# Kernel tuning notes

Measured on AMD Instinct MI355X. Metric: run time of the kernel, lower is better.

Reference implementation:

```python
import jax, jax.numpy as jnp
import numpy as np
from jax import lax

EPS = 1e-5
B, NV, NP, C = 1, 12000, 32, 5
VF = 128            # voxel_feat_dim
OF = 256            # output_feat_dim
D0, H0, W0 = 16, 128, 128


def _bn(x, gamma, beta, axes):
    # training-mode batch norm (biased variance), channel dim broadcasts via gamma/beta shape
    mean = jnp.mean(x, axis=axes, keepdims=True)
    var = jnp.var(x, axis=axes, keepdims=True)
    return (x - mean) * lax.rsqrt(var + EPS) * gamma + beta


def _vfe(x, w, b, gamma, beta):
    # x: (B, NVox, NPts, Cin) -> (B, NVox, Cout); linear -> BN1d over all rows -> relu -> max over points
    y = jnp.einsum('bvpc,co->bvpo', x, w) + b
    Bv, Nv, Pp, Co = y.shape
    y = _bn(y.reshape(Bv * Nv * Pp, Co), gamma, beta, axes=0).reshape(Bv, Nv, Pp, Co)
    y = jax.nn.relu(y)
    return jnp.max(y, axis=2)


def _conv_bn_relu(x, w, b, gamma, beta):
    y = lax.conv_general_dilated(x, w, (2, 2, 2), [(1, 1)] * 3,
                                 dimension_numbers=('NCDHW', 'OIDHW', 'NCDHW'))
    y = y + b[None, :, None, None, None]
    y = _bn(y, gamma[None, :, None, None, None], beta[None, :, None, None, None], axes=(0, 2, 3, 4))
    return jax.nn.relu(y)


def setup_inputs() -> dict:
    key = jax.random.key(0)
    ks = jax.random.split(key, 20)
    vf = VF // 2
    inp = {
        'voxel_features': jax.random.normal(ks[0], (B, NV, NP, C), jnp.float32),
        'voxel_coords': jnp.stack([
            jax.random.randint(ks[1], (B, NV), 0, D0),
            jax.random.randint(ks[2], (B, NV), 0, H0),
            jax.random.randint(ks[3], (B, NV), 0, W0)], axis=-1).astype(jnp.int32),
        'grid_d': D0, 'grid_h': H0, 'grid_w': W0,
        # VFE1: 5 -> 64
        'w1': jax.random.normal(ks[4], (C, vf), jnp.float32) * 0.05,
        'b1': jnp.zeros((vf,), jnp.float32),
        'g1': jnp.ones((vf,), jnp.float32),
        'be1': jnp.zeros((vf,), jnp.float32),
        # VFE2: 64 -> 128
        'w2': jax.random.normal(ks[5], (vf, VF), jnp.float32) * 0.05,
        'b2': jnp.zeros((VF,), jnp.float32),
        'g2': jnp.ones((VF,), jnp.float32),
        'be2': jnp.zeros((VF,), jnp.float32),
        # conv3d stack
        'cw1': jax.random.normal(ks[6], (128, VF, 3, 3, 3), jnp.float32) * 0.02,
        'cb1': jnp.zeros((128,), jnp.float32),
        'cg1': jnp.ones((128,), jnp.float32),
        'cbe1': jnp.zeros((128,), jnp.float32),
        'cw2': jax.random.normal(ks[7], (256, 128, 3, 3, 3), jnp.float32) * 0.02,
        'cb2': jnp.zeros((256,), jnp.float32),
        'cg2': jnp.ones((256,), jnp.float32),
        'cbe2': jnp.zeros((256,), jnp.float32),
        'cw3': jax.random.normal(ks[8], (OF, 256, 3, 3, 3), jnp.float32) * 0.02,
        'cb3': jnp.zeros((OF,), jnp.float32),
        'cg3': jnp.ones((OF,), jnp.float32),
        'cbe3': jnp.zeros((OF,), jnp.float32),
    }
    return inp


def reference(voxel_features, voxel_coords, grid_d, grid_h, grid_w,
              w1, b1, g1, be1, w2, b2, g2, be2,
              cw1, cb1, cg1, cbe1, cw2, cb2, cg2, cbe2, cw3, cb3, cg3, cbe3):
    # VFE1: (B, NV, NP, C) -> (B, NV, 64)
    f = _vfe(voxel_features, w1, b1, g1, be1)
    # VFE2 (repaired: singleton points dim, max over 1 point is identity)
    f = _vfe(f[:, :, None, :], w2, b2, g2, be2)  # (B, NV, 128)

    Bn, Nn, Cf = f.shape
    grid = jnp.zeros((Bn, grid_d, grid_h, grid_w, Cf), f.dtype)
    bidx = jnp.broadcast_to(jnp.arange(Bn)[:, None], (Bn, Nn))
    grid = grid.at[bidx, voxel_coords[..., 0], voxel_coords[..., 1], voxel_coords[..., 2]].set(f)
    grid = jnp.transpose(grid, (0, 4, 1, 2, 3))  # (B, Cf, D, H, W)

    x = _conv_bn_relu(grid, cw1, cb1, cg1, cbe1)
    x = _conv_bn_relu(x, cw2, cb2, cg2, cbe2)
    x = _conv_bn_relu(x, cw3, cb3, cg3, cbe3)
    return x
```

## Files before the change

### kernel.cpp

```cpp
#include <hip/hip_runtime.h>

#define NVOX 12000
#define NPTS 32
#define CIN  5
#define C1   64
#define C2   128
#define GD   16
#define GH   128
#define GW   128
#define SP   (GD*GH*GW)
static constexpr float EPSBN = 1e-5f;

typedef unsigned short ushortT;
typedef __attribute__((ext_vector_type(8))) short bf16x8;
typedef __attribute__((ext_vector_type(4))) float f32x4;

__device__ inline ushortT f2bf(float f) {
    unsigned int x = __float_as_uint(f);
    unsigned int r = (x + 0x7FFFu + ((x >> 16) & 1u)) >> 16;
    return (ushortT)r;
}
__device__ inline float bf2f(ushortT u) { return __uint_as_float(((unsigned int)u) << 16); }

__device__ inline void gload16(const ushortT* g, ushortT* l) {
    __builtin_amdgcn_global_load_lds(
        (const __attribute__((address_space(1))) unsigned int*)g,
        (__attribute__((address_space(3))) unsigned int*)l, 16, 0, 0);
}

#define P1D 18
#define P1H 130
#define P1W 130
#define PSP1 (P1D*P1H*P1W)
#define P2D 10
#define P2H 66
#define P2W 66
#define PSP2 (P2D*P2H*P2W)
#define P3D 6
#define P3H 34
#define P3W 34
#define PSP3 (P3D*P3H*P3W)


__device__ inline void conv_w_one(const float* cw, ushortT* wb, int CI_, int TCO_,
                                  int NS_, int e) {
    int j = e & 7;
    int rest = e >> 3;
    int CHN = TCO_*16;
    int p = rest % CHN; int r = rest / CHN;
    int s = r % NS_;    int cob = r / NS_;
    int col = p >> 4, cp = p & 15;
    int cl = cp ^ (col & 7);
    int tap = (CI_==256) ? (s>>1) : s;
    int cib = (CI_==256) ? ((s&1)*128) : 0;
    int co = cob*TCO_ + col;
    int ci = cib + cl*8 + j;
    wb[e] = f2bf(cw[((size_t)co*CI_ + ci)*27 + tap]);
}

__global__ void prep(const float* __restrict__ x, const float* __restrict__ w1,
                     float* __restrict__ s1sum,
                     const float* __restrict__ cw1, const float* __restrict__ cw2,
                     const float* __restrict__ cw3, ushortT* __restrict__ wb1,
                     ushortT* __restrict__ wb2, ushortT* __restrict__ wb3,
                     const int* __restrict__ coords, int* __restrict__ winner) {
    __shared__ float s_w[CIN*C1];
    __shared__ float s_red[2][4][C1];
    const int blk = blockIdx.x;
    const int t = threadIdx.x;
    if (blk < 960) {
        for (int i = t; i < CIN*C1; i += 256) s_w[i] = w1[i];
        __syncthreads();
        int ch = t & 63, rr = t >> 6;
        float sum = 0.f, sq = 0.f;
        const int NROWS = NVOX * NPTS;
        for (int row = blk*4 + rr; row < NROWS; row += 960*4) {
            const float* xr = x + row*CIN;
            float y = 0.f;
            #pragma unroll
            for (int c = 0; c < CIN; ++c) y += xr[c] * s_w[c*C1 + ch];
            sum += y; sq += y*y;
        }
        s_red[0][rr][ch] = sum; s_red[1][rr][ch] = sq;
        __syncthreads();
        if (rr == 0) {
            sum = s_red[0][0][ch]+s_red[0][1][ch]+s_red[0][2][ch]+s_red[0][3][ch];
            sq  = s_red[1][0][ch]+s_red[1][1][ch]+s_red[1][2][ch]+s_red[1][3][ch];
            atomicAdd(&s1sum[ch], sum);
            atomicAdd(&s1sum[C1+ch], sq);
        }
    } else if (blk < 1984) {
        const int N1 = 442368, N2 = 884736, N3 = 1769472;
        const int total = N1+N2+N3;
        for (int e0 = (blk-960)*256 + t; e0 < total; e0 += 1024*256) {
            if (e0 < N1)         conv_w_one(cw1, wb1, 128, 128, 27, e0);
            else if (e0 < N1+N2) conv_w_one(cw2, wb2, 128, 128, 27, e0-N1);
            else                 conv_w_one(cw3, wb3, 256, 64,  54, e0-N1-N2);
        }
    } else {
        int v = (blk-1984)*256 + t;
        if (v < NVOX) {
            int d = coords[v*3+0], h = coords[v*3+1], w = coords[v*3+2];
            atomicMax(&winner[(d*GH + h)*GW + w], v);
        }
    }
}

__global__ void vfe1_apply(const float* __restrict__ x, const float* __restrict__ w1,
                           const float* __restrict__ sums, const float* __restrict__ g,
                           const float* __restrict__ be, float* __restrict__ f1) {
    __shared__ float s_w[CIN*C1];
    __shared__ float s_x[4*NPTS*CIN];
    int v0 = blockIdx.x*4, t = threadIdx.x;
    for (int i = t; i < CIN*C1; i += 256) s_w[i] = w1[i];
    for (int i = t; i < 4*NPTS*CIN; i += 256) s_x[i] = x[(size_t)v0*NPTS*CIN + i];
    int sub = t >> 6, ch = t & 63;
    const float invN = 1.f/(NVOX*NPTS);
    float mean = sums[ch]*invN;
    float var  = sums[C1+ch]*invN - mean*mean;
    float sc = g[ch]*rsqrtf(var + EPSBN);
    float sh = be[ch] - mean*sc;
    __syncthreads();
    float m = 0.f;
    const float* xs = s_x + sub*NPTS*CIN;
    for (int p = 0; p < NPTS; ++p) {
        float y = 0.f;
        #pragma unroll
        for (int c = 0; c < CIN; ++c) y += xs[p*CIN+c]*s_w[c*C1+ch];
        m = fmaxf(m, y*sc + sh);
    }
    f1[(v0+sub)*C1 + ch] = m;
}

__global__ void vfe2_linear(const float* __restrict__ f1, const float* __restrict__ w2,
                            float* __restrict__ y2, float* __restrict__ sums) {
    __shared__ float s_w[C2][68];
    __shared__ float s_f[16*C1];
    int t = threadIdx.x;
    for (int i = t; i < C1*C2; i += 128) {
        int c = i >> 7, o = i & 127;
        s_w[o][c] = w2[i];
    }
    int v0 = blockIdx.x*16;
    for (int i = t; i < 16*C1; i += 128) s_f[i] = f1[v0*C1 + i];
    __syncthreads();
    float sum = 0.f, sq = 0.f;
    for (int vl = 0; vl < 16; ++vl) {
        float y = 0.f;
        #pragma unroll
        for (int c4 = 0; c4 < C1; c4 += 4) {
            float4 f = *(const float4*)&s_f[vl*C1 + c4];
            float4 w = *(const float4*)&s_w[t][c4];
            y += f.x*w.x + f.y*w.y + f.z*w.z + f.w*w.w;
        }
        y2[(v0+vl)*C2 + t] = y;
        sum += y; sq += y*y;
    }
    atomicAdd(&sums[t], sum);
    atomicAdd(&sums[C2+t], sq);
}

__global__ void vfe2_apply_bf16(const float* __restrict__ y2, const float* __restrict__ sums,
                                const float* __restrict__ g, const float* __restrict__ be,
                                ushortT* __restrict__ f2b) {
    __shared__ float s_sc[C2], s_sh[C2];
    int t = threadIdx.x;
    if (t < C2) {
        const float invN = 1.f/NVOX;
        float mean = sums[t]*invN;
        float var  = sums[C2+t]*invN - mean*mean;
        float sc = g[t]*rsqrtf(var + EPSBN);
        s_sc[t] = sc; s_sh[t] = be[t] - mean*sc;
    }
    __syncthreads();
    int i = blockIdx.x*256 + t;
    if (i >= NVOX*C2/4) return;
    const float4 v = *(const float4*)(y2 + (size_t)i*4);
    int c0 = (i*4) & (C2-1);
    ushort4 o;
    o.x = f2bf(fmaxf(0.f, v.x*s_sc[c0+0]+s_sh[c0+0]));
    o.y = f2bf(fmaxf(0.f, v.y*s_sc[c0+1]+s_sh[c0+1]));
    o.z = f2bf(fmaxf(0.f, v.z*s_sc[c0+2]+s_sh[c0+2]));
    o.w = f2bf(fmaxf(0.f, v.w*s_sc[c0+3]+s_sh[c0+3]));
    *(ushort4*)(f2b + (size_t)i*4) = o;
}

__global__ void build_grid_cl(const int* __restrict__ winner, const ushortT* __restrict__ f2b,
                              ushortT* __restrict__ grid) {
    const int total = PSP1*16;
    for (int e = blockIdx.x*256 + threadIdx.x; e < total; e += gridDim.x*256) {
        int pos = e >> 4, ch = e & 15;
        int pz = pos / (P1H*P1W); int rr = pos % (P1H*P1W);
        int py = rr / P1W; int px = rr % P1W;
        unsigned dz = pz-1, dy = py-1, dx = px-1;
        int4 v = {0,0,0,0};
        if (dz < GD && dy < GH && dx < GW) {
            int wn_ = winner[(dz*GH + dy)*GW + dx];
            if (wn_ >= 0) v = *(const int4*)(f2b + (size_t)wn_*C2 + ch*8);
        }
        *(int4*)(grid + ((size_t)pos << 7) + ch*8) = v;
    }
}

template<int CI, int CO, int TILE_CO, int TILE_SP, int THREADS,
         int PD, int PH, int PW, int DO, int HO, int WO,
         int OPH, int OPW, int NS, int NSLICE, bool ATOMIC>
__global__ __launch_bounds__(THREADS) void conv3d_mfma(
        const ushortT* __restrict__ in_p, const ushortT* __restrict__ wb,
        void* __restrict__ outp, float* __restrict__ sums_out) {
    constexpr int NW      = THREADS/64;
    constexpr int WAVES_M = TILE_CO/32;
    constexpr int WAVES_N = NW/WAVES_M;
    constexpr int FRAG_N  = TILE_SP/(WAVES_N*16);
    constexpr int TILE_Y  = TILE_SP/8;
    constexpr int SPB     = NS/NSLICE;
    constexpr int WCH     = TILE_CO*16;

    __shared__ ushortT s_x[2][TILE_SP*128];
    __shared__ ushortT s_w[2][TILE_CO*128];

    constexpr int nbx = WO/8, nby = HO/TILE_Y;
    constexpr int NWG = nbx*nby*DO*(CO/TILE_CO)*NSLICE;
    int b = (blockIdx.x & 7)*(NWG >> 3) + (blockIdx.x >> 3);
    const int bx = b % nbx; b /= nbx;
    const int by = b % nby; b /= nby;
    const int bz = b % DO;  b /= DO;
    const int cob   = b % (CO/TILE_CO);
    const int slice = b / (CO/TILE_CO);
    const int co0 = cob*TILE_CO;
    const int oy0 = by*TILE_Y, ox0 = bx*8;
    const int t = threadIdx.x;
    const int lane = t & 63, wid = t >> 6;
    const int lr = lane & 15, lq = lane >> 4;
    const int wm = wid % WAVES_M, wn = wid / WAVES_M;

    size_t xpre[4];
    #pragma unroll
    for (int j = 0; j < 4; ++j) {
        int q = t + j*THREADS;
        int n = q >> 4, cp = q & 15;
        int cl = cp ^ (n & 7);
        int oy = n >> 3, ox = n & 7;
        xpre[j] = (size_t)(((2*bz)*PH + (2*oy0 + 2*oy))*PW + (2*ox0 + 2*ox))*CI + cl*8;
    }
    int aoff[2], axr[2], boff[FRAG_N], bxr[FRAG_N];
    #pragma unroll
    for (int f = 0; f < 2; ++f) {
        int c = wm*32 + f*16 + lr;
        aoff[f] = c*128; axr[f] = c & 7;
    }
    #pragma unroll
    for (int f = 0; f < FRAG_N; ++f) {
        int n = wn*(FRAG_N*16) + f*16 + lr;
        boff[f] = n*128; bxr[f] = n & 7;
    }

    f32x4 acc[2][FRAG_N];
    #pragma unroll
    for (int i = 0; i < 2; ++i)
        #pragma unroll
        for (int j = 0; j < FRAG_N; ++j) acc[i][j] = (f32x4){0.f,0.f,0.f,0.f};

    const int s0 = slice*SPB;

#define STAGE(bufi, s) { \
    const int tap_ = (CI==256) ? ((s)>>1) : (s); \
    const int cib_ = (CI==256) ? (((s)&1)*128) : 0; \
    const int kz_ = tap_/9, ky_ = (tap_/3)%3, kx_ = tap_%3; \
    const ushortT* wsrc_ = wb + ((size_t)(cob*NS + (s)))*(WCH*8); \
    _Pragma("unroll") for (int j = 0; j < 4; ++j) \
        gload16(wsrc_ + (size_t)(t + j*THREADS)*8, &s_w[bufi][(wid*64 + j*THREADS)*8]); \
    const size_t koff_ = (size_t)((kz_*PH + ky_)*PW + kx_)*CI + cib_; \
    _Pragma("unroll") for (int j = 0; j < 4; ++j) \
        gload16(in_p + xpre[j] + koff_, &s_x[bufi][(wid*64 + j*THREADS)*8]); }

#define COMPUTE(bufi) { \
    _Pragma("unroll") for (int ks = 0; ks < 4; ++ks) { \
        int cl_ = ks*4 + lq; \
        bf16x8 a0 = *(const bf16x8*)&s_w[bufi][aoff[0] + ((cl_ ^ axr[0])<<3)]; \
        bf16x8 a1 = *(const bf16x8*)&s_w[bufi][aoff[1] + ((cl_ ^ axr[1])<<3)]; \
        _Pragma("unroll") for (int f = 0; f < FRAG_N; ++f) { \
            bf16x8 bf = *(const bf16x8*)&s_x[bufi][boff[f] + ((cl_ ^ bxr[f])<<3)]; \
            acc[0][f] = __builtin_amdgcn_mfma_f32_16x16x32_bf16(a0, bf, acc[0][f],0,0,0); \
            acc[1][f] = __builtin_amdgcn_mfma_f32_16x16x32_bf16(a1, bf, acc[1][f],0,0,0); } } }

    STAGE(0, s0);
    __syncthreads();
    #pragma unroll
    for (int ph = 0; ph < SPB; ++ph) {
        const int buf = ph & 1;
        if (ph + 1 < SPB) STAGE(buf^1, s0 + ph + 1);
        COMPUTE(buf);
        __syncthreads();
    }
#undef STAGE
#undef COMPUTE

    if constexpr (!ATOMIC) {
        ushortT* out = (ushortT*)outp;
        #pragma unroll
        for (int fm = 0; fm < 2; ++fm)
        #pragma unroll
        for (int fn = 0; fn < FRAG_N; ++fn) {
            int n = wn*(FRAG_N*16) + fn*16 + lr;
            int oy = n >> 3, ox = n & 7;
            int c_ = co0 + wm*32 + fm*16 + lq*4;
            size_t pa = ((size_t)(bz+1)*OPH + (oy0+oy+1))*OPW + (ox0+ox+1);
            ushort4 o;
            o.x = f2bf(acc[fm][fn][0]); o.y = f2bf(acc[fm][fn][1]);
            o.z = f2bf(acc[fm][fn][2]); o.w = f2bf(acc[fm][fn][3]);
            *(ushort4*)(out + pa*CO + c_) = o;
        }
        #pragma unroll
        for (int fm = 0; fm < 2; ++fm) {
            float sv[4], qv[4];
            #pragma unroll
            for (int r = 0; r < 4; ++r) {
                float ssum = 0.f, qsum = 0.f;
                #pragma unroll
                for (int fn = 0; fn < FRAG_N; ++fn) {
                    float a = acc[fm][fn][r]; ssum += a; qsum += a*a;
                }
                #pragma unroll
                for (int m = 1; m < 16; m <<= 1) {
                    ssum += __shfl_xor(ssum, m, 64);
                    qsum += __shfl_xor(qsum, m, 64);
                }
                sv[r] = ssum; qv[r] = qsum;
            }
            if (lr == 0) {
                int c_ = co0 + wm*32 + fm*16 + lq*4;
                #pragma unroll
                for (int r = 0; r < 4; ++r) {
                    atomicAdd(&sums_out[c_+r], sv[r]);
                    atomicAdd(&sums_out[CO + c_+r], qv[r]);
                }
            }
        }
    } else {
        float* out = (float*)outp;
        #pragma unroll
        for (int fm = 0; fm < 2; ++fm)
        #pragma unroll
        for (int fn = 0; fn < FRAG_N; ++fn) {
            int n = wn*(FRAG_N*16) + fn*16 + lr;
            int oy = n >> 3, ox = n & 7;
            int c_ = co0 + wm*32 + fm*16 + lq*4;
            #pragma unroll
            for (int r = 0; r < 4; ++r)
                atomicAdd(&out[((size_t)(c_+r)*DO + bz)*(HO*WO) + (oy0+oy)*WO + ox0+ox],
                          acc[fm][fn][r]);
        }
    }
}

template<int C, int PD, int PH, int PW>
__global__ void bn_apply_pad(ushortT* __restrict__ y, const float* __restrict__ sums,
                             const float* __restrict__ g, const float* __restrict__ be,
                             float invN) {
    constexpr int CH = C/8;
    constexpr int total = PD*PH*PW*CH;
    __shared__ float s_sc[C], s_sh[C];
    for (int c = threadIdx.x; c < C; c += 256) {
        float mean = sums[c]*invN;
        float var  = sums[C+c]*invN - mean*mean;
        float sc = g[c]*rsqrtf(var + EPSBN);
        s_sc[c] = sc; s_sh[c] = be[c] - mean*sc;
    }
    __syncthreads();
    for (int e = blockIdx.x*256 + threadIdx.x; e < total; e += gridDim.x*256) {
        int pos = e / CH;
        int c0 = (e % CH)*8;
        int pz = pos / (PH*PW); int rr = pos % (PH*PW);
        int py = rr / PW; int px = rr % PW;
        if ((unsigned)(pz-1) >= (unsigned)(PD-2) || (unsigned)(py-1) >= (unsigned)(PH-2) ||
            (unsigned)(px-1) >= (unsigned)(PW-2)) continue;
        ushortT* p = y + (size_t)pos*C + c0;
        ushort4 a = *(ushort4*)p, b4 = *(ushort4*)(p+4);
        ushort4 o1, o2;
        o1.x = f2bf(fmaxf(0.f, bf2f(a.x)*s_sc[c0+0]+s_sh[c0+0]));
        o1.y = f2bf(fmaxf(0.f, bf2f(a.y)*s_sc[c0+1]+s_sh[c0+1]));
        o1.z = f2bf(fmaxf(0.f, bf2f(a.z)*s_sc[c0+2]+s_sh[c0+2]));
        o1.w = f2bf(fmaxf(0.f, bf2f(a.w)*s_sc[c0+3]+s_sh[c0+3]));
        o2.x = f2bf(fmaxf(0.f, bf2f(b4.x)*s_sc[c0+4]+s_sh[c0+4]));
        o2.y = f2bf(fmaxf(0.f, bf2f(b4.y)*s_sc[c0+5]+s_sh[c0+5]));
        o2.z = f2bf(fmaxf(0.f, bf2f(b4.z)*s_sc[c0+6]+s_sh[c0+6]));
        o2.w = f2bf(fmaxf(0.f, bf2f(b4.w)*s_sc[c0+7]+s_sh[c0+7]));
        *(ushort4*)p     = o1;
        *(ushort4*)(p+4) = o2;
    }
}

template<int SPL>
__global__ void bn_stats_cmajor(const float* __restrict__ y, const float* __restrict__ g,
                                const float* __restrict__ be, float* __restrict__ ss, int C) {
    __shared__ float s_red[2][256];
    int c = blockIdx.x;
    const float* p = y + (size_t)c*SPL;
    float sum = 0.f, sq = 0.f;
    for (int i = threadIdx.x; i < SPL; i += 256) { float v = p[i]; sum += v; sq += v*v; }
    s_red[0][threadIdx.x] = sum; s_red[1][threadIdx.x] = sq;
    __syncthreads();
    for (int s = 128; s > 0; s >>= 1) {
        if (threadIdx.x < s) {
            s_red[0][threadIdx.x] += s_red[0][threadIdx.x+s];
            s_red[1][threadIdx.x] += s_red[1][threadIdx.x+s];
        }
        __syncthreads();
    }
    if (threadIdx.x == 0) {
        float invN = 1.f/(float)SPL;
        float mean = s_red[0][0]*invN;
        float var  = s_red[1][0]*invN - mean*mean;
        float sc = g[c]*rsqrtf(var + EPSBN);
        ss[c] = sc; ss[C+c] = be[c] - mean*sc;
    }
}

template<int LOGSPL>
__global__ void bn_apply_cmajor(float* __restrict__ y, const float* __restrict__ ss,
                                int C, int total) {
    for (int i = blockIdx.x*blockDim.x + threadIdx.x; i < total; i += gridDim.x*blockDim.x) {
        int c = i >> LOGSPL;
        y[i] = fmaxf(0.f, y[i]*ss[c] + ss[C+c]);
    }
}

extern "C" void kernel_launch(void* const* d_in, const int* in_sizes, int n_in,
                              void* d_out, int out_size, void* d_ws, size_t ws_size,
                              hipStream_t stream) {
    const float* x      = (const float*)d_in[0];
    const int*   coords = (const int*)  d_in[1];
    const float* w1  = (const float*)d_in[5];
    const float* g1  = (const float*)d_in[7];
    const float* be1 = (const float*)d_in[8];
    const float* w2  = (const float*)d_in[9];
    const float* g2  = (const float*)d_in[11];
    const float* be2 = (const float*)d_in[12];
    const float* cw1 = (const float*)d_in[13];
    const float* cg1 = (const float*)d_in[15];
    const float* cbe1= (const float*)d_in[16];
    const float* cw2 = (const float*)d_in[17];
    const float* cg2 = (const float*)d_in[19];
    const float* cbe2= (const float*)d_in[20];
    const float* cw3 = (const float*)d_in[21];
    const float* cg3 = (const float*)d_in[23];
    const float* cbe3= (const float*)d_in[24];
    float* out = (float*)d_out;

    float*   ws     = (float*)d_ws;
    float*   stats  = ws;
    int*     winner = (int*)(ws + 4096);
    float*   f1     = (float*)(winner + SP);
    float*   y2     = f1 + (size_t)NVOX*C1;
    ushortT* f2b    = (ushortT*)(y2 + (size_t)NVOX*C2);
    ushortT* grid   = f2b + (size_t)NVOX*C2;
    ushortT* c1o    = grid + (size_t)PSP1*128;
    ushortT* c2o    = c1o + (size_t)PSP2*128;
    ushortT* wb1    = c2o + (size_t)PSP3*256;
    ushortT* wb2    = wb1 + 442368;
    ushortT* wb3    = wb2 + 884736;

    float* s1sum = stats;
    float* s2sum = stats + 128;
    float* c1sum = stats + 384;
    float* c2sum = stats + 640;
    float* ss3   = stats + 1152;

    hipMemsetAsync(stats, 0, 4096*sizeof(float), stream);
    hipMemsetAsync(winner, 0xFF, SP*sizeof(int), stream);
    hipMemsetAsync(c1o, 0, (size_t)PSP2*128*2, stream);
    hipMemsetAsync(c2o, 0, (size_t)PSP3*256*2, stream);
    hipMemsetAsync(d_out, 0, (size_t)out_size*sizeof(float), stream);

    prep<<<2031, 256, 0, stream>>>(x, w1, s1sum, cw1, cw2, cw3, wb1, wb2, wb3,
                                   coords, winner);
    vfe1_apply<<<NVOX/4, 256, 0, stream>>>(x, w1, s1sum, g1, be1, f1);
    vfe2_linear<<<NVOX/16, 128, 0, stream>>>(f1, w2, y2, s2sum);
    vfe2_apply_bf16<<<NVOX*C2/4/256, 256, 0, stream>>>(y2, s2sum, g2, be2, f2b);
    build_grid_cl<<<4096, 256, 0, stream>>>(winner, f2b, grid);

    conv3d_mfma<128,128, 128,128,512, P1D,P1H,P1W, 8,64,64, P2H,P2W, 27,1,false>
        <<<8*4*8, 512, 0, stream>>>(grid, wb1, c1o, c1sum);
    bn_apply_pad<128, P2D,P2H,P2W><<<1024, 256, 0, stream>>>(c1o, c1sum, cg1, cbe1,
                                                             1.f/32768.f);
    conv3d_mfma<128,256, 128,128,512, P2D,P2H,P2W, 4,32,32, P3H,P3W, 27,1,false>
        <<<4*2*4*2, 512, 0, stream>>>(c1o, wb2, c2o, c2sum);
    bn_apply_pad<256, P3D,P3H,P3W><<<512, 256, 0, stream>>>(c2o, c2sum, cg2, cbe2,
                                                            1.f/4096.f);
    conv3d_mfma<256,256, 64,64,256, P3D,P3H,P3W, 2,16,16, 1,1, 54,6,true>
        <<<2*2*2*4*6, 256, 0, stream>>>(c2o, wb3, (void*)out, nullptr);

    bn_stats_cmajor<2*16*16><<<256, 256, 0, stream>>>(out, cg3, cbe3, ss3, 256);
    bn_apply_cmajor<9><<<512, 256, 0, stream>>>(out, ss3, 256, 131072);
}
```

Measured before the change: 290.4 us.

## Gather sparse voxel features directly in conv1 instead of materializing dense grid

Removes the build_grid_cl kernel that wrote a padded dense bf16 grid of about 77 MB. The first conv now loads a halo of winner indices into shared memory and gathers feature rows straight from the voxel feature buffer, pointing empty cells at a zero buffer. This cuts a large write and re-read of mostly-zero memory, at the cost of an indirect load per stage. The second conv also moves to 64x64 tiles with 256 threads and more workgroups, and its weight packing is updated to match.

```diff
diff --git a/kernel.cpp b/kernel.cpp
--- a/kernel.cpp
+++ b/kernel.cpp
@@ -28,10 +28,6 @@
         (__attribute__((address_space(3))) unsigned int*)l, 16, 0, 0);
 }
 
-#define P1D 18
-#define P1H 130
-#define P1W 130
-#define PSP1 (P1D*P1H*P1W)
 #define P2D 10
 #define P2H 66
 #define P2W 66
@@ -94,7 +90,7 @@
         const int total = N1+N2+N3;
         for (int e0 = (blk-960)*256 + t; e0 < total; e0 += 1024*256) {
             if (e0 < N1)         conv_w_one(cw1, wb1, 128, 128, 27, e0);
-            else if (e0 < N1+N2) conv_w_one(cw2, wb2, 128, 128, 27, e0-N1);
+            else if (e0 < N1+N2) conv_w_one(cw2, wb2, 128, 64,  27, e0-N1);
             else                 conv_w_one(cw3, wb3, 256, 64,  54, e0-N1-N2);
         }
     } else {
@@ -185,29 +181,13 @@
     *(ushort4*)(f2b + (size_t)i*4) = o;
 }
 
-__global__ void build_grid_cl(const int* __restrict__ winner, const ushortT* __restrict__ f2b,
-                              ushortT* __restrict__ grid) {
-    const int total = PSP1*16;
-    for (int e = blockIdx.x*256 + threadIdx.x; e < total; e += gridDim.x*256) {
-        int pos = e >> 4, ch = e & 15;
-        int pz = pos / (P1H*P1W); int rr = pos % (P1H*P1W);
-        int py = rr / P1W; int px = rr % P1W;
-        unsigned dz = pz-1, dy = py-1, dx = px-1;
-        int4 v = {0,0,0,0};
-        if (dz < GD && dy < GH && dx < GW) {
-            int wn_ = winner[(dz*GH + dy)*GW + dx];
-            if (wn_ >= 0) v = *(const int4*)(f2b + (size_t)wn_*C2 + ch*8);
-        }
-        *(int4*)(grid + ((size_t)pos << 7) + ch*8) = v;
-    }
-}
-
 template<int CI, int CO, int TILE_CO, int TILE_SP, int THREADS,
          int PD, int PH, int PW, int DO, int HO, int WO,
-         int OPH, int OPW, int NS, int NSLICE, bool ATOMIC>
+         int OPH, int OPW, int NS, int NSLICE, bool ATOMIC, bool GATHER>
 __global__ __launch_bounds__(THREADS) void conv3d_mfma(
         const ushortT* __restrict__ in_p, const ushortT* __restrict__ wb,
-        void* __restrict__ outp, float* __restrict__ sums_out) {
+        void* __restrict__ outp, float* __restrict__ sums_out,
+        const int* __restrict__ winner, const ushortT* __restrict__ zerop) {
     constexpr int NW      = THREADS/64;
     constexpr int WAVES_M = TILE_CO/32;
     constexpr int WAVES_N = NW/WAVES_M;
@@ -215,9 +195,11 @@
     constexpr int TILE_Y  = TILE_SP/8;
     constexpr int SPB     = NS/NSLICE;
     constexpr int WCH     = TILE_CO*16;
+    constexpr int NHALO   = 3*(2*TILE_Y+1)*17;
 
     __shared__ ushortT s_x[2][TILE_SP*128];
     __shared__ ushortT s_w[2][TILE_CO*128];
+    __shared__ short   s_wn[GATHER ? NHALO : 2];
 
     constexpr int nbx = WO/8, nby = HO/TILE_Y;
     constexpr int NWG = nbx*nby*DO*(CO/TILE_CO)*NSLICE;
@@ -234,14 +216,35 @@
     const int lr = lane & 15, lq = lane >> 4;
     const int wm = wid % WAVES_M, wn = wid / WAVES_M;
 
-    size_t xpre[4];
+    if constexpr (GATHER) {
+        constexpr int HROW = 2*TILE_Y+1;
+        for (int c = t; c < NHALO; c += THREADS) {
+            int zz = c/(HROW*17), rr = c%(HROW*17), yy = rr/17, xx = rr%17;
+            int iz = 2*bz-1+zz, iy = 2*oy0-1+yy, ix = 2*ox0-1+xx;
+            int wv = -1;
+            if ((unsigned)iz < (unsigned)GD && (unsigned)iy < (unsigned)GH &&
+                (unsigned)ix < (unsigned)GW)
+                wv = winner[(iz*GH + iy)*GW + ix];
+            s_wn[c] = (short)wv;
+        }
+        __syncthreads();
+    }
+
+    size_t xpre[4]; int xbase[4]; int cl8[4];
     #pragma unroll
     for (int j = 0; j < 4; ++j) {
         int q = t + j*THREADS;
         int n = q >> 4, cp = q & 15;
         int cl = cp ^ (n & 7);
         int oy = n >> 3, ox = n & 7;
-        xpre[j] = (size_t)(((2*bz)*PH + (2*oy0 + 2*oy))*PW + (2*ox0 + 2*ox))*CI + cl*8;
+        if constexpr (GATHER) {
+            xbase[j] = (2*oy)*17 + 2*ox;
+            cl8[j]   = cl*8;
+            xpre[j]  = 0;
+        } else {
+            xpre[j] = (size_t)(((2*bz)*PH + (2*oy0 + 2*oy))*PW + (2*ox0 + 2*ox))*CI + cl*8;
+            xbase[j] = 0; cl8[j] = 0;
+        }
     }
     int aoff[2], axr[2], boff[FRAG_N], bxr[FRAG_N];
     #pragma unroll
@@ -270,9 +273,18 @@
     const ushortT* wsrc_ = wb + ((size_t)(cob*NS + (s)))*(WCH*8); \
     _Pragma("unroll") for (int j = 0; j < 4; ++j) \
         gload16(wsrc_ + (size_t)(t + j*THREADS)*8, &s_w[bufi][(wid*64 + j*THREADS)*8]); \
-    const size_t koff_ = (size_t)((kz_*PH + ky_)*PW + kx_)*CI + cib_; \
-    _Pragma("unroll") for (int j = 0; j < 4; ++j) \
-        gload16(in_p + xpre[j] + koff_, &s_x[bufi][(wid*64 + j*THREADS)*8]); }
+    if constexpr (GATHER) { \
+        const int poff_ = kz_*((2*TILE_Y+1)*17) + ky_*17 + kx_; \
+        _Pragma("unroll") for (int j = 0; j < 4; ++j) { \
+            int wv_ = s_wn[xbase[j] + poff_]; \
+            const ushortT* src_ = (wv_ >= 0) ? in_p + ((size_t)wv_ << 7) + cl8[j] : zerop; \
+            gload16(src_, &s_x[bufi][(wid*64 + j*THREADS)*8]); \
+        } \
+    } else { \
+        const size_t koff_ = (size_t)((kz_*PH + ky_)*PW + kx_)*CI + cib_; \
+        _Pragma("unroll") for (int j = 0; j < 4; ++j) \
+            gload16(in_p + xpre[j] + koff_, &s_x[bufi][(wid*64 + j*THREADS)*8]); \
+    } }
 
 #define COMPUTE(bufi) { \
     _Pragma("unroll") for (int ks = 0; ks < 4; ++ks) { \
@@ -454,8 +466,7 @@
     float*   f1     = (float*)(winner + SP);
     float*   y2     = f1 + (size_t)NVOX*C1;
     ushortT* f2b    = (ushortT*)(y2 + (size_t)NVOX*C2);
-    ushortT* grid   = f2b + (size_t)NVOX*C2;
-    ushortT* c1o    = grid + (size_t)PSP1*128;
+    ushortT* c1o    = f2b + (size_t)NVOX*C2;
     ushortT* c2o    = c1o + (size_t)PSP2*128;
     ushortT* wb1    = c2o + (size_t)PSP3*256;
     ushortT* wb2    = wb1 + 442368;
@@ -466,6 +477,7 @@
     float* c1sum = stats + 384;
     float* c2sum = stats + 640;
     float* ss3   = stats + 1152;
+    const ushortT* zerop = (const ushortT*)(stats + 2048);
 
     hipMemsetAsync(stats, 0, 4096*sizeof(float), stream);
     hipMemsetAsync(winner, 0xFF, SP*sizeof(int), stream);
@@ -478,18 +490,17 @@
     vfe1_apply<<<NVOX/4, 256, 0, stream>>>(x, w1, s1sum, g1, be1, f1);
     vfe2_linear<<<NVOX/16, 128, 0, stream>>>(f1, w2, y2, s2sum);
     vfe2_apply_bf16<<<NVOX*C2/4/256, 256, 0, stream>>>(y2, s2sum, g2, be2, f2b);
-    build_grid_cl<<<4096, 256, 0, stream>>>(winner, f2b, grid);
-
-    conv3d_mfma<128,128, 128,128,512, P1D,P1H,P1W, 8,64,64, P2H,P2W, 27,1,false>
-        <<<8*4*8, 512, 0, stream>>>(grid, wb1, c1o, c1sum);
+
+    conv3d_mfma<128,128, 128,128,512, 1,1,1, 8,64,64, P2H,P2W, 27,1,false,true>
+        <<<8*4*8, 512, 0, stream>>>(f2b, wb1, c1o, c1sum, winner, zerop);
     bn_apply_pad<128, P2D,P2H,P2W><<<1024, 256, 0, stream>>>(c1o, c1sum, cg1, cbe1,
                                                              1.f/32768.f);
-    conv3d_mfma<128,256, 128,128,512, P2D,P2H,P2W, 4,32,32, P3H,P3W, 27,1,false>
-        <<<4*2*4*2, 512, 0, stream>>>(c1o, wb2, c2o, c2sum);
+    conv3d_mfma<128,256, 64,64,256, P2D,P2H,P2W, 4,32,32, P3H,P3W, 27,1,false,false>
+        <<<4*4*4*4, 256, 0, stream>>>(c1o, wb2, c2o, c2sum, nullptr, nullptr);
     bn_apply_pad<256, P3D,P3H,P3W><<<512, 256, 0, stream>>>(c2o, c2sum, cg2, cbe2,
                                                             1.f/4096.f);
-    conv3d_mfma<256,256, 64,64,256, P3D,P3H,P3W, 2,16,16, 1,1, 54,6,true>
-        <<<2*2*2*4*6, 256, 0, stream>>>(c2o, wb3, (void*)out, nullptr);
+    conv3d_mfma<256,256, 64,64,256, P3D,P3H,P3W, 2,16,16, 1,1, 54,6,true,false>
+        <<<2*2*2*4*6, 256, 0, stream>>>(c2o, wb3, (void*)out, nullptr, nullptr, nullptr);
 
     bn_stats_cmajor<2*16*16><<<256, 256, 0, stream>>>(out, cg3, cbe3, ss3, 256);
     bn_apply_cmajor<9><<<512, 256, 0, stream>>>(out, ss3, 256, 131072);
```

Result: faster. 266.9 us (-8.1%).
